# Kernel tuning notes

Hardware: AMD Instinct MI355X
Metric: run time of the kernel (lower is better)

Reference implementation:

```python
import jax, jax.numpy as jnp
import numpy as np

B, S, I, H, O, L = 64, 1024, 512, 512, 512, 3


def setup_inputs() -> dict:
    key = jax.random.key(0)
    ks = jax.random.split(key, 14)
    sc = 0.05  # small init to avoid gate saturation
    inp = {
        "input": jax.random.normal(ks[0], (B, S, I), jnp.float32),
        "hidden_state": jax.random.normal(ks[1], (B, L, H), jnp.float32),
        # gate params; x-side Linear has bias, h-side has none (as in torch module)
        "Wzx": jax.random.normal(ks[2], (L, I, H), jnp.float32) * sc,
        "bzx": jnp.zeros((L, H), jnp.float32),
        "Wzh": jax.random.normal(ks[3], (L, H, H), jnp.float32) * sc,
        "Wrx": jax.random.normal(ks[4], (L, I, H), jnp.float32) * sc,
        "brx": jnp.zeros((L, H), jnp.float32),
        "Wrh": jax.random.normal(ks[5], (L, H, H), jnp.float32) * sc,
        "Wgx": jax.random.normal(ks[6], (L, I, H), jnp.float32) * sc,
        "bgx": jnp.zeros((L, H), jnp.float32),
        "Wgh": jax.random.normal(ks[7], (L, H, H), jnp.float32) * sc,
        "Wout": jax.random.normal(ks[8], (H, O), jnp.float32) * sc,
        "bout": jnp.zeros((O,), jnp.float32),
    }
    return inp


def reference(input, hidden_state, Wzx, bzx, Wzh, Wrx, brx, Wrh, Wgx, bgx, Wgh, Wout, bout):
    n_layers = Wzx.shape[0]
    Bn = input.shape[0]
    Hn = hidden_state.shape[2]
    # layer_states: n_layers initial states + one extra zeros slot (matches torch code)
    states0 = jnp.concatenate(
        [jnp.transpose(hidden_state, (1, 0, 2)),
         jnp.zeros((1, Bn, Hn), input.dtype)], axis=0)  # (L+1, B, H)

    def step(states, x_t):
        x = x_t  # (B, I)
        for l in range(n_layers):
            # NOTE: faithfully reproduces the original's indexing: layer l reads
            # states[l], which for l>=1 was just overwritten by layer l-1 this step.
            h = states[l]
            z = jax.nn.sigmoid(x @ Wzx[l] + bzx[l] + h @ Wzh[l])
            r = jax.nn.sigmoid(x @ Wrx[l] + brx[l] + h @ Wrh[l])
            g = jnp.tanh(x @ Wgx[l] + bgx[l] + (r * h) @ Wgh[l])
            h = z * h + (1.0 - z) * g
            x = h  # dropout=0 -> identity
            states = states.at[l + 1].set(h)
        out_t = x @ Wout + bout  # (B, O)
        return states, out_t

    states_f, outs = jax.lax.scan(step, states0, jnp.transpose(input, (1, 0, 2)))
    layer_output = jnp.transpose(outs, (1, 0, 2))          # (B, S, O)
    hidden_out = jnp.transpose(states_f[:n_layers], (1, 0, 2))  # (B, L, H)
    return layer_output, hidden_out
```

## Files before the change

### kernel.cpp

```cpp
#include <hip/hip_runtime.h>


typedef __attribute__((ext_vector_type(4))) float f32x4;
typedef __attribute__((ext_vector_type(8))) __bf16 bf16x8;

#define NROWS 65536
#define HID_OFF 33554432ull

__device__ __forceinline__ void gload16(const void* g, void* l) {
  __builtin_amdgcn_global_load_lds((const __attribute__((address_space(1))) void*)g,
                                   (__attribute__((address_space(3))) void*)l,
                                   16, 0, 0);
}
__device__ __forceinline__ float sigmoidf_(float x) { return 1.f / (1.f + __expf(-x)); }
__device__ __forceinline__ float tanh_fast(float x) {
  const float e = __expf(2.f * x);
  return 1.f - 2.f / (e + 1.f);
}

__device__ __forceinline__ void stage32(const __bf16* __restrict__ src, int k0,
                                        __bf16* lds, int w, int lane) {
#pragma unroll
  for (int i = 0; i < 2; ++i) {
    const int s0 = (w * 2 + i) * 64;
    const int s = s0 + lane;
    const int row = s >> 2;
    const int cc = (s ^ row) & 3;
    gload16(src + (size_t)row * 512 + k0 + cc * 8, lds + s0 * 8);
  }
}

__device__ __forceinline__ bf16x8 frag32(const __bf16* t, int row, int lane) {
  const int c = ((lane >> 4) ^ row) & 3;
  return *(const bf16x8*)(t + row * 32 + c * 8);
}

__device__ __forceinline__ void stage_ht(const __bf16* __restrict__ src,
                                         __bf16* Ht, int w, int lane) {
#pragma unroll
  for (int i = 0; i < 8; ++i) {
    const int s0 = i * 256 + w * 64;
    const int s = s0 + lane;
    const int row = s >> 4, cc = s & 15;
    gload16(src + (size_t)row * 512 + cc * 8, Ht + s0 * 8);
  }
  asm volatile("s_waitcnt vmcnt(0)");
  __builtin_amdgcn_sched_barrier(0);
  __builtin_amdgcn_s_barrier();
  __builtin_amdgcn_sched_barrier(0);
}

template<int EPI, bool L0>
__global__ __launch_bounds__(256, 4) void gemm7(
    const __bf16* __restrict__ A,
    const __bf16* __restrict__ Bt,
    int tiles_n, int row_off,
    const float* __restrict__ bias,
    const float* __restrict__ cterm,
    const float* __restrict__ h0f,
    const __bf16* __restrict__ haux,
    const __bf16* __restrict__ zf,
    const __bf16* __restrict__ gf,
    __bf16* __restrict__ o_rh,
    __bf16* __restrict__ o_h,
    float* __restrict__ o_f)
{
  __shared__ alignas(16) __bf16 smem[16384];
  __bf16* const A0 = smem;
  __bf16* const B0 = smem + 4096;
  __bf16* const A1 = smem + 8192;
  __bf16* const B1 = smem + 12288;

  const int tid = threadIdx.x, lane = tid & 63, w = tid >> 6;

  int bid = blockIdx.x;
  {
    const int nwg = gridDim.x;
    const int q = nwg >> 3, r = nwg & 7;
    const int x = bid & 7, rest = bid >> 3;
    bid = (x < r ? x * (q + 1) : r * (q + 1) + (x - r) * q) + rest;
  }
  const int tm = bid / tiles_n;
  const int tn = bid - tm * tiles_n;
  const size_t arow0 = (size_t)tm * 128;
  const int brow0 = tn * 128;
  const __bf16* const Ab = A + arow0 * 512;
  const __bf16* const Bb = Bt + (size_t)brow0 * 512;

  const int wr = (w >> 1) * 64;
  const int wc = (w & 1) * 64;

  f32x4 acc[4][4];
  const f32x4 zz = {0.f, 0.f, 0.f, 0.f};
#pragma unroll
  for (int i = 0; i < 4; ++i)
#pragma unroll
    for (int j = 0; j < 4; ++j) acc[i][j] = zz;

  auto step = [&](int t, const __bf16* cA, const __bf16* cB,
                  __bf16* nA, __bf16* nB) {
    if (t < 15) {
      stage32(Ab, (t + 1) * 32, nA, w, lane);
      stage32(Bb, (t + 1) * 32, nB, w, lane);
    }
    bf16x8 af[4], bb4[4];
#pragma unroll
    for (int i = 0; i < 4; ++i) {
      af[i]  = frag32(cA, wr + i * 16 + (lane & 15), lane);
      bb4[i] = frag32(cB, wc + i * 16 + (lane & 15), lane);
    }
#pragma unroll
    for (int mi = 0; mi < 4; ++mi)
#pragma unroll
      for (int ni = 0; ni < 4; ++ni)
        acc[mi][ni] = __builtin_amdgcn_mfma_f32_16x16x32_bf16(af[mi], bb4[ni], acc[mi][ni], 0, 0, 0);
    if (t < 15) {
      asm volatile("s_waitcnt vmcnt(0)");
      __builtin_amdgcn_sched_barrier(0);
    }
    __builtin_amdgcn_sched_barrier(0);
    __builtin_amdgcn_s_barrier();
    __builtin_amdgcn_sched_barrier(0);
  };

  stage32(Ab, 0, A0, w, lane);
  stage32(Bb, 0, B0, w, lane);
  asm volatile("s_waitcnt vmcnt(0)");
  __builtin_amdgcn_sched_barrier(0);
  __builtin_amdgcn_s_barrier();
  __builtin_amdgcn_sched_barrier(0);

#pragma unroll 1
  for (int t = 0; t < 16; t += 2) {
    step(t,     A0, B0, A1, B1);
    step(t + 1, A1, B1, A0, B0);
  }

  const int fcol = lane & 15;
  const int frow = (lane >> 4) * 4;
  const int bb0 = (row_off + (int)arow0) >> 10;

  if (EPI == 0) {
    if (tn < 4) {
      const size_t foff = ((size_t)(tm * 4 + tn)) * 16384 + (size_t)tid * 64;
      __bf16* zw = (__bf16*)zf;
#pragma unroll
      for (int mi = 0; mi < 4; ++mi) {
        bf16x8 p0, p1;
#pragma unroll
        for (int ni = 0; ni < 4; ++ni)
#pragma unroll
          for (int j = 0; j < 4; ++j) {
            const int gcol = brow0 + wc + ni * 16 + fcol;
            float c = acc[mi][ni][j] + bias[gcol];
            if (L0) c += cterm[bb0 * 1024 + gcol];
            const float v = sigmoidf_(c);
            const int idx = ni * 4 + j;
            if (idx < 8) p0[idx] = (__bf16)v; else p1[idx - 8] = (__bf16)v;
          }
        *(bf16x8*)(zw + foff + mi * 16) = p0;
        *(bf16x8*)(zw + foff + mi * 16 + 8) = p1;
      }
    } else if (tn < 8) {
      if (!L0) stage_ht(haux + arow0 * 512 + (tn - 4) * 128, smem, w, lane);
#pragma unroll
      for (int mi = 0; mi < 4; ++mi)
#pragma unroll
        for (int ni = 0; ni < 4; ++ni)
#pragma unroll
          for (int j = 0; j < 4; ++j) {
            const int rloc = (int)arow0 + wr + mi * 16 + frow + j;
            const int gcol = brow0 + wc + ni * 16 + fcol;
            const int nn = gcol - 512;
            float c = acc[mi][ni][j] + bias[gcol];
            if (L0) c += cterm[bb0 * 1024 + gcol];
            const float rv = sigmoidf_(c);
            const float h = L0 ? h0f[bb0 * 1536 + nn]
                               : (float)smem[(wr + mi * 16 + frow + j) * 128 + wc + ni * 16 + fcol];
            o_rh[(size_t)rloc * 512 + nn] = (__bf16)(rv * h);
          }
    } else {
      const size_t foff = ((size_t)(tm * 4 + (tn - 8))) * 16384 + (size_t)tid * 64;
      __bf16* gw = (__bf16*)gf;
#pragma unroll
      for (int mi = 0; mi < 4; ++mi) {
        bf16x8 p0, p1;
#pragma unroll
        for (int ni = 0; ni < 4; ++ni)
#pragma unroll
          for (int j = 0; j < 4; ++j) {
            const int gcol = brow0 + wc + ni * 16 + fcol;
            const float v = acc[mi][ni][j] + bias[gcol];
            const int idx = ni * 4 + j;
            if (idx < 8) p0[idx] = (__bf16)v; else p1[idx - 8] = (__bf16)v;
          }
        *(bf16x8*)(gw + foff + mi * 16) = p0;
        *(bf16x8*)(gw + foff + mi * 16 + 8) = p1;
      }
    }
  } else if (EPI == 1) {
    if (!L0) stage_ht(haux + arow0 * 512 + tn * 128, smem, w, lane);
    const size_t foff = ((size_t)(tm * 4 + tn)) * 16384 + (size_t)tid * 64;
    const bool has_last = (o_f != nullptr) && ((tm & 7) == 7);
#pragma unroll
    for (int mi = 0; mi < 4; ++mi) {
      const bf16x8 z0 = *(const bf16x8*)(zf + foff + mi * 16);
      const bf16x8 z1 = *(const bf16x8*)(zf + foff + mi * 16 + 8);
      const bf16x8 g0 = *(const bf16x8*)(gf + foff + mi * 16);
      const bf16x8 g1 = *(const bf16x8*)(gf + foff + mi * 16 + 8);
#pragma unroll
      for (int ni = 0; ni < 4; ++ni)
#pragma unroll
        for (int j = 0; j < 4; ++j) {
          const int rloc = (int)arow0 + wr + mi * 16 + frow + j;
          const int gcol = brow0 + wc + ni * 16 + fcol;
          const int idx = ni * 4 + j;
          const float zv = (float)(idx < 8 ? z0[idx] : z1[idx - 8]);
          const float gp = (float)(idx < 8 ? g0[idx] : g1[idx - 8]);
          const float gv = tanh_fast(gp + acc[mi][ni][j]);
          const float h = L0 ? h0f[bb0 * 1536 + gcol]
                             : (float)smem[(wr + mi * 16 + frow + j) * 128 + wc + ni * 16 + fcol];
          const float hv = zv * h + (1.f - zv) * gv;
          o_h[(size_t)rloc * 512 + gcol] = (__bf16)hv;
          if (has_last && ((rloc & 1023) == 1023))
            o_f[(size_t)bb0 * 1536 + gcol] = (float)(__bf16)hv;
        }
    }
  } else {
#pragma unroll
    for (int mi = 0; mi < 4; ++mi)
#pragma unroll
      for (int ni = 0; ni < 4; ++ni)
#pragma unroll
        for (int j = 0; j < 4; ++j) {
          const int rloc = (int)arow0 + wr + mi * 16 + frow + j;
          const int gcol = brow0 + wc + ni * 16 + fcol;
          o_f[(size_t)rloc * 512 + gcol] = acc[mi][ni][j] + bias[gcol];
        }
  }
}


__global__ void prep_pack(const float* __restrict__ Wzx, const float* __restrict__ Wzh,
                          const float* __restrict__ Wrx, const float* __restrict__ Wrh,
                          const float* __restrict__ Wgx, const float* __restrict__ Wgh,
                          const float* __restrict__ Wout,
                          __bf16* __restrict__ W1t, __bf16* __restrict__ Wght,
                          __bf16* __restrict__ Woutt)
{
  const int slot = blockIdx.z;
  const float* srcA;
  const float* srcB = nullptr;
  __bf16* dst;
  if (slot < 9) {
    const int l = slot / 3, g = slot % 3;
    srcA = (g == 0 ? Wzx : g == 1 ? Wrx : Wgx) + (size_t)l * 512 * 512;
    if (l > 0 && g < 2) srcB = (g == 0 ? Wzh : Wrh) + (size_t)l * 512 * 512;
    dst = W1t + (size_t)l * 1536 * 512 + (size_t)g * 512 * 512;
  } else if (slot < 12) {
    const int l = slot - 9;
    srcA = Wgh + (size_t)l * 512 * 512;
    dst = Wght + (size_t)l * 512 * 512;
  } else {
    srcA = Wout;
    dst = Woutt;
  }
  __shared__ float tile[32][33];
  const int k0 = blockIdx.x * 32;
  const int n0 = blockIdx.y * 32;
  const int tx = threadIdx.x;
  const int ty = threadIdx.y;
  for (int i = ty; i < 32; i += 8) {
    float v = srcA[(size_t)(k0 + i) * 512 + n0 + tx];
    if (srcB) v += srcB[(size_t)(k0 + i) * 512 + n0 + tx];
    tile[i][tx] = v;
  }
  __syncthreads();
  for (int i = ty; i < 32; i += 8)
    dst[(size_t)(n0 + i) * 512 + k0 + tx] = (__bf16)tile[tx][i];
}

__global__ void cterm_kernel(const float* __restrict__ hidden,
                             const float* __restrict__ Wzh,
                             const float* __restrict__ Wrh,
                             float* __restrict__ Cterm)
{
  const int idx = blockIdx.x * blockDim.x + threadIdx.x;
  const int b = idx >> 10;
  const int n = idx & 1023;
  const float* W = (n < 512 ? Wzh : Wrh);
  const int nn = n & 511;
  const float* h0 = hidden + (size_t)b * 1536;
  float acc = 0.f;
  for (int k = 0; k < 512; ++k) acc += h0[k] * W[(size_t)k * 512 + nn];
  Cterm[idx] = acc;
}

__global__ void small_prep(const float* __restrict__ bzx, const float* __restrict__ brx,
                           const float* __restrict__ bgx, const float* __restrict__ hidden,
                           float* __restrict__ bias1, float* __restrict__ out_hidden)
{
  const int idx = blockIdx.x * blockDim.x + threadIdx.x;
  if (idx < 3 * 1536) {
    const int l = idx / 1536, j = idx % 1536;
    const float* src = (j < 512 ? bzx : j < 1024 ? brx : bgx);
    bias1[idx] = src[l * 512 + (j & 511)];
  }
  const int hidx = idx - 3 * 1536;
  if (hidx >= 0 && hidx < 64 * 512) {
    const int b = hidx >> 9, n = hidx & 511;
    out_hidden[(size_t)b * 1536 + n] = hidden[(size_t)b * 1536 + n];
  }
}

__global__ void convert_x(const float* __restrict__ src, __bf16* __restrict__ dst, long n)
{
  const long i = ((long)blockIdx.x * blockDim.x + threadIdx.x) * 8;
  if (i >= n) return;
  const f32x4 a = *(const f32x4*)(src + i);
  const f32x4 b = *(const f32x4*)(src + i + 4);
  bf16x8 o;
  o[0] = (__bf16)a[0]; o[1] = (__bf16)a[1]; o[2] = (__bf16)a[2]; o[3] = (__bf16)a[3];
  o[4] = (__bf16)b[0]; o[5] = (__bf16)b[1]; o[6] = (__bf16)b[2]; o[7] = (__bf16)b[3];
  *(bf16x8*)(dst + i) = o;
}

extern "C" void kernel_launch(void* const* d_in, const int* in_sizes, int n_in,
                              void* d_out, int out_size, void* d_ws, size_t ws_size,
                              hipStream_t stream) {
  const float* input  = (const float*)d_in[0];
  const float* hidden = (const float*)d_in[1];
  const float* Wzx = (const float*)d_in[2];
  const float* bzx = (const float*)d_in[3];
  const float* Wzh = (const float*)d_in[4];
  const float* Wrx = (const float*)d_in[5];
  const float* brx = (const float*)d_in[6];
  const float* Wrh = (const float*)d_in[7];
  const float* Wgx = (const float*)d_in[8];
  const float* bgx = (const float*)d_in[9];
  const float* Wgh = (const float*)d_in[10];
  const float* Wout = (const float*)d_in[11];
  const float* bout = (const float*)d_in[12];

  float* out = (float*)d_out;
  float* out_hidden = out + HID_OFF;

  char* ws = (char*)d_ws;
  size_t off = 0;
  auto carve = [&](size_t bytes) -> void* {
    off = (off + 255) & ~(size_t)255;
    void* p = ws + off;
    off += bytes;
    return p;
  };

  __bf16* W1t   = (__bf16*)carve(3ull * 1536 * 512 * 2);
  __bf16* Wght  = (__bf16*)carve(3ull * 512 * 512 * 2);
  __bf16* Woutt = (__bf16*)carve(512ull * 512 * 2);
  float*  bias1 = (float*) carve(3ull * 1536 * 4);
  float*  Cterm = (float*) carve(64ull * 1024 * 4);
  const size_t fixed_end = off;

  long chunk_rows = NROWS;
  int C = 1;
  while (C < 32) {
    const size_t need = ((fixed_end + 255) & ~(size_t)255) +
                        5ull * (size_t)chunk_rows * 512 * 2 + 5 * 256;
    if (need <= ws_size) break;
    C *= 2;
    chunk_rows /= 2;
  }
  __bf16* bufA  = (__bf16*)carve((size_t)chunk_rows * 512 * 2);
  __bf16* bufB  = (__bf16*)carve((size_t)chunk_rows * 512 * 2);
  __bf16* zfrag = (__bf16*)carve((size_t)chunk_rows * 512 * 2);
  __bf16* rhb   = (__bf16*)carve((size_t)chunk_rows * 512 * 2);
  __bf16* gfrag = (__bf16*)carve((size_t)chunk_rows * 512 * 2);

  small_prep<<<(3 * 1536 + 64 * 512 + 255) / 256, 256, 0, stream>>>(
      bzx, brx, bgx, hidden, bias1, out_hidden);
  dim3 tp_grid(16, 16, 13), tp_blk(32, 8);
  prep_pack<<<tp_grid, tp_blk, 0, stream>>>(Wzx, Wzh, Wrx, Wrh, Wgx, Wgh, Wout,
                                            W1t, Wght, Woutt);
  cterm_kernel<<<65536 / 256, 256, 0, stream>>>(hidden, Wzh, Wrh, Cterm);

  for (int c = 0; c < C; ++c) {
    const long row_off = (long)c * chunk_rows;
    const long nelem = chunk_rows * 512;
    const int mt = (int)(chunk_rows / 128);

    convert_x<<<(int)((nelem / 8 + 255) / 256), 256, 0, stream>>>(
        input + (size_t)row_off * 512, bufA, nelem);

    gemm7<0, true><<<mt * 12, 256, 0, stream>>>(
        bufA, W1t, 12, (int)row_off, bias1, Cterm, hidden, nullptr,
        zfrag, gfrag, rhb, nullptr, nullptr);
    gemm7<1, true><<<mt * 4, 256, 0, stream>>>(
        rhb, Wght, 4, (int)row_off, nullptr, nullptr, hidden, nullptr,
        zfrag, gfrag, nullptr, bufB, out_hidden + 512);

    gemm7<0, false><<<mt * 12, 256, 0, stream>>>(
        bufB, W1t + 1536 * 512, 12, (int)row_off, bias1 + 1536, nullptr, nullptr, bufB,
        zfrag, gfrag, rhb, nullptr, nullptr);
    gemm7<1, false><<<mt * 4, 256, 0, stream>>>(
        rhb, Wght + 512 * 512, 4, (int)row_off, nullptr, nullptr, nullptr, bufB,
        zfrag, gfrag, nullptr, bufA, out_hidden + 1024);

    gemm7<0, false><<<mt * 12, 256, 0, stream>>>(
        bufA, W1t + 2 * 1536 * 512, 12, (int)row_off, bias1 + 3072, nullptr, nullptr, bufA,
        zfrag, gfrag, rhb, nullptr, nullptr);
    gemm7<1, false><<<mt * 4, 256, 0, stream>>>(
        rhb, Wght + 2 * 512 * 512, 4, (int)row_off, nullptr, nullptr, nullptr, bufA,
        zfrag, gfrag, nullptr, bufB, nullptr);

    gemm7<2, false><<<mt * 4, 256, 0, stream>>>(
        bufB, Woutt, 4, (int)row_off, bout, nullptr, nullptr, nullptr,
        nullptr, nullptr, nullptr, nullptr, out + (size_t)row_off * 512);
  }
}
```

Before: 927.5 us.

## Triple-buffer GEMM K-loop with two-ahead prefetch and new LDS swizzle

Replaces the double-buffered LDS staging in the bf16 MFMA GEMM with a three-buffer ring that prefetches two K-slices ahead and waits with vmcnt(4) rather than draining all loads every step. The XOR swizzle for the A/B tiles now uses row>>1 to change the LDS bank pattern. The EPI==1 epilogue issues its z/g fragment loads before staging the hidden tile, so those loads overlap. In exchange, LDS use grows from 32KB to 48KB per block and launch bounds drop to 3 blocks per CU, which lowers occupancy.

After: 863.1 us (median of 3 runs). -6.9%, faster.

```diff
diff --git a/kernel.cpp b/kernel.cpp
--- a/kernel.cpp
+++ b/kernel.cpp
@@ -25,13 +25,13 @@
     const int s0 = (w * 2 + i) * 64;
     const int s = s0 + lane;
     const int row = s >> 2;
-    const int cc = (s ^ row) & 3;
+    const int cc = ((s & 3) ^ (row >> 1)) & 3;
     gload16(src + (size_t)row * 512 + k0 + cc * 8, lds + s0 * 8);
   }
 }
 
 __device__ __forceinline__ bf16x8 frag32(const __bf16* t, int row, int lane) {
-  const int c = ((lane >> 4) ^ row) & 3;
+  const int c = (((lane >> 4) ^ (row >> 1)) & 3);
   return *(const bf16x8*)(t + row * 32 + c * 8);
 }
 
@@ -51,7 +51,7 @@
 }
 
 template<int EPI, bool L0>
-__global__ __launch_bounds__(256, 4) void gemm7(
+__global__ __launch_bounds__(256, 3) void gemm9(
     const __bf16* __restrict__ A,
     const __bf16* __restrict__ Bt,
     int tiles_n, int row_off,
@@ -65,11 +65,13 @@
     __bf16* __restrict__ o_h,
     float* __restrict__ o_f)
 {
-  __shared__ alignas(16) __bf16 smem[16384];
+  __shared__ alignas(16) __bf16 smem[24576];
   __bf16* const A0 = smem;
   __bf16* const B0 = smem + 4096;
   __bf16* const A1 = smem + 8192;
   __bf16* const B1 = smem + 12288;
+  __bf16* const A2 = smem + 16384;
+  __bf16* const B2 = smem + 20480;
 
   const int tid = threadIdx.x, lane = tid & 63, w = tid >> 6;
 
@@ -97,11 +99,11 @@
 #pragma unroll
     for (int j = 0; j < 4; ++j) acc[i][j] = zz;
 
-  auto step = [&](int t, const __bf16* cA, const __bf16* cB,
-                  __bf16* nA, __bf16* nB) {
-    if (t < 15) {
-      stage32(Ab, (t + 1) * 32, nA, w, lane);
-      stage32(Bb, (t + 1) * 32, nB, w, lane);
+  auto stepf = [&](int t, const __bf16* cA, const __bf16* cB,
+                   __bf16* nA, __bf16* nB, int vm) {
+    if (nA) {
+      stage32(Ab, (t + 2) * 32, nA, w, lane);
+      stage32(Bb, (t + 2) * 32, nB, w, lane);
     }
     bf16x8 af[4], bb4[4];
 #pragma unroll
@@ -114,27 +116,37 @@
 #pragma unroll
       for (int ni = 0; ni < 4; ++ni)
         acc[mi][ni] = __builtin_amdgcn_mfma_f32_16x16x32_bf16(af[mi], bb4[ni], acc[mi][ni], 0, 0, 0);
-    if (t < 15) {
+    if (vm == 4) {
+      asm volatile("s_waitcnt vmcnt(4)");
+      __builtin_amdgcn_sched_barrier(0);
+    } else if (vm == 0) {
       asm volatile("s_waitcnt vmcnt(0)");
       __builtin_amdgcn_sched_barrier(0);
     }
-    __builtin_amdgcn_sched_barrier(0);
     __builtin_amdgcn_s_barrier();
     __builtin_amdgcn_sched_barrier(0);
   };
 
   stage32(Ab, 0, A0, w, lane);
   stage32(Bb, 0, B0, w, lane);
-  asm volatile("s_waitcnt vmcnt(0)");
+  stage32(Ab, 32, A1, w, lane);
+  stage32(Bb, 32, B1, w, lane);
+  asm volatile("s_waitcnt vmcnt(4)");
   __builtin_amdgcn_sched_barrier(0);
   __builtin_amdgcn_s_barrier();
   __builtin_amdgcn_sched_barrier(0);
 
 #pragma unroll 1
-  for (int t = 0; t < 16; t += 2) {
-    step(t,     A0, B0, A1, B1);
-    step(t + 1, A1, B1, A0, B0);
-  }
+  for (int it = 0; it < 4; ++it) {
+    const int t = it * 3;
+    stepf(t,     A0, B0, A2, B2, 4);
+    stepf(t + 1, A1, B1, A0, B0, 4);
+    stepf(t + 2, A2, B2, A1, B1, 4);
+  }
+  stepf(12, A0, B0, A2, B2, 4);
+  stepf(13, A1, B1, A0, B0, 4);
+  stepf(14, A2, B2, nullptr, nullptr, 0);
+  stepf(15, A0, B0, nullptr, nullptr, -1);
 
   const int fcol = lane & 15;
   const int frow = (lane >> 4) * 4;
@@ -199,15 +211,19 @@
       }
     }
   } else if (EPI == 1) {
+    const size_t foff = ((size_t)(tm * 4 + tn)) * 16384 + (size_t)tid * 64;
+    bf16x8 zr[4][2], gr[4][2];
+#pragma unroll
+    for (int mi = 0; mi < 4; ++mi) {
+      zr[mi][0] = *(const bf16x8*)(zf + foff + mi * 16);
+      zr[mi][1] = *(const bf16x8*)(zf + foff + mi * 16 + 8);
+      gr[mi][0] = *(const bf16x8*)(gf + foff + mi * 16);
+      gr[mi][1] = *(const bf16x8*)(gf + foff + mi * 16 + 8);
+    }
     if (!L0) stage_ht(haux + arow0 * 512 + tn * 128, smem, w, lane);
-    const size_t foff = ((size_t)(tm * 4 + tn)) * 16384 + (size_t)tid * 64;
     const bool has_last = (o_f != nullptr) && ((tm & 7) == 7);
 #pragma unroll
     for (int mi = 0; mi < 4; ++mi) {
-      const bf16x8 z0 = *(const bf16x8*)(zf + foff + mi * 16);
-      const bf16x8 z1 = *(const bf16x8*)(zf + foff + mi * 16 + 8);
-      const bf16x8 g0 = *(const bf16x8*)(gf + foff + mi * 16);
-      const bf16x8 g1 = *(const bf16x8*)(gf + foff + mi * 16 + 8);
 #pragma unroll
       for (int ni = 0; ni < 4; ++ni)
 #pragma unroll
@@ -215,8 +231,8 @@
           const int rloc = (int)arow0 + wr + mi * 16 + frow + j;
           const int gcol = brow0 + wc + ni * 16 + fcol;
           const int idx = ni * 4 + j;
-          const float zv = (float)(idx < 8 ? z0[idx] : z1[idx - 8]);
-          const float gp = (float)(idx < 8 ? g0[idx] : g1[idx - 8]);
+          const float zv = (float)(idx < 8 ? zr[mi][0][idx] : zr[mi][1][idx - 8]);
+          const float gp = (float)(idx < 8 ? gr[mi][0][idx] : gr[mi][1][idx - 8]);
           const float gv = tanh_fast(gp + acc[mi][ni][j]);
           const float h = L0 ? h0f[bb0 * 1536 + gcol]
                              : (float)smem[(wr + mi * 16 + frow + j) * 128 + wc + ni * 16 + fcol];
@@ -391,28 +407,28 @@
     convert_x<<<(int)((nelem / 8 + 255) / 256), 256, 0, stream>>>(
         input + (size_t)row_off * 512, bufA, nelem);
 
-    gemm7<0, true><<<mt * 12, 256, 0, stream>>>(
+    gemm9<0, true><<<mt * 12, 256, 0, stream>>>(
         bufA, W1t, 12, (int)row_off, bias1, Cterm, hidden, nullptr,
         zfrag, gfrag, rhb, nullptr, nullptr);
-    gemm7<1, true><<<mt * 4, 256, 0, stream>>>(
+    gemm9<1, true><<<mt * 4, 256, 0, stream>>>(
         rhb, Wght, 4, (int)row_off, nullptr, nullptr, hidden, nullptr,
         zfrag, gfrag, nullptr, bufB, out_hidden + 512);
 
-    gemm7<0, false><<<mt * 12, 256, 0, stream>>>(
+    gemm9<0, false><<<mt * 12, 256, 0, stream>>>(
         bufB, W1t + 1536 * 512, 12, (int)row_off, bias1 + 1536, nullptr, nullptr, bufB,
         zfrag, gfrag, rhb, nullptr, nullptr);
-    gemm7<1, false><<<mt * 4, 256, 0, stream>>>(
+    gemm9<1, false><<<mt * 4, 256, 0, stream>>>(
         rhb, Wght + 512 * 512, 4, (int)row_off, nullptr, nullptr, nullptr, bufB,
         zfrag, gfrag, nullptr, bufA, out_hidden + 1024);
 
-    gemm7<0, false><<<mt * 12, 256, 0, stream>>>(
+    gemm9<0, false><<<mt * 12, 256, 0, stream>>>(
         bufA, W1t + 2 * 1536 * 512, 12, (int)row_off, bias1 + 3072, nullptr, nullptr, bufA,
         zfrag, gfrag, rhb, nullptr, nullptr);
-    gemm7<1, false><<<mt * 4, 256, 0, stream>>>(
+    gemm9<1, false><<<mt * 4, 256, 0, stream>>>(
         rhb, Wght + 2 * 512 * 512, 4, (int)row_off, nullptr, nullptr, nullptr, bufA,
         zfrag, gfrag, nullptr, bufB, nullptr);
 
-    gemm7<2, false><<<mt * 4, 256, 0, stream>>>(
+    gemm9<2, false><<<mt * 4, 256, 0, stream>>>(
         bufB, Woutt, 4, (int)row_off, bout, nullptr, nullptr, nullptr,
         nullptr, nullptr, nullptr, nullptr, out + (size_t)row_off * 512);
   }
```

## Use 256x256 tiles with 16-wave blocks, triple-buffered LDS, and h-fragment passthrough

Applied to the files above, without the earlier changes.

Replaces the 128x128 GEMM tile with 256 threads by a 256x256 tile computed by 1024 threads, with a three-stage LDS pipeline that waits on vmcnt(2) to keep two K-slices in flight. The r-gate epilogue now stages h through LDS in two passes and writes h in fragment order to a new hfrag buffer, so the update GEMM reads h directly instead of restaging it from global memory. The goal is higher operand reuse per loaded byte and less epilogue staging, at the cost of one block per CU, 96KB LDS per block, fewer blocks in total (possible wave-quantisation and occupancy loss), and an extra workspace buffer.

After: 1.312 ms. 41.5% more time.

```diff
diff --git a/kernel.cpp b/kernel.cpp
--- a/kernel.cpp
+++ b/kernel.cpp
@@ -18,28 +18,24 @@
   return 1.f - 2.f / (e + 1.f);
 }
 
-__device__ __forceinline__ void stage32(const __bf16* __restrict__ src, int k0,
-                                        __bf16* lds, int w, int lane) {
-#pragma unroll
-  for (int i = 0; i < 2; ++i) {
-    const int s0 = (w * 2 + i) * 64;
-    const int s = s0 + lane;
-    const int row = s >> 2;
-    const int cc = (s ^ row) & 3;
-    gload16(src + (size_t)row * 512 + k0 + cc * 8, lds + s0 * 8);
-  }
+__device__ __forceinline__ void stage256(const __bf16* __restrict__ src, int k0,
+                                         __bf16* lds, int w, int lane) {
+  const int s = w * 64 + lane;
+  const int row = s >> 2;
+  const int cc = ((s & 3) ^ (row >> 1)) & 3;
+  gload16(src + (size_t)row * 512 + k0 + cc * 8, lds + (w * 64) * 8);
 }
 
 __device__ __forceinline__ bf16x8 frag32(const __bf16* t, int row, int lane) {
-  const int c = ((lane >> 4) ^ row) & 3;
+  const int c = (((lane >> 4) ^ (row >> 1)) & 3);
   return *(const bf16x8*)(t + row * 32 + c * 8);
 }
 
-__device__ __forceinline__ void stage_ht(const __bf16* __restrict__ src,
-                                         __bf16* Ht, int w, int lane) {
-#pragma unroll
-  for (int i = 0; i < 8; ++i) {
-    const int s0 = i * 256 + w * 64;
+__device__ __forceinline__ void stage_ht256(const __bf16* __restrict__ src,
+                                            __bf16* Ht, int w, int lane) {
+#pragma unroll
+  for (int i = 0; i < 4; ++i) {
+    const int s0 = i * 1024 + w * 64;
     const int s = s0 + lane;
     const int row = s >> 4, cc = s & 15;
     gload16(src + (size_t)row * 512 + cc * 8, Ht + s0 * 8);
@@ -51,7 +47,7 @@
 }
 
 template<int EPI, bool L0>
-__global__ __launch_bounds__(256, 4) void gemm7(
+__global__ __launch_bounds__(1024, 1) void gemm14(
     const __bf16* __restrict__ A,
     const __bf16* __restrict__ Bt,
     int tiles_n, int row_off,
@@ -61,17 +57,21 @@
     const __bf16* __restrict__ haux,
     const __bf16* __restrict__ zf,
     const __bf16* __restrict__ gf,
+    const __bf16* __restrict__ hf,
     __bf16* __restrict__ o_rh,
     __bf16* __restrict__ o_h,
     float* __restrict__ o_f)
 {
-  __shared__ alignas(16) __bf16 smem[16384];
+  __shared__ alignas(16) __bf16 smem[49152];
   __bf16* const A0 = smem;
-  __bf16* const B0 = smem + 4096;
-  __bf16* const A1 = smem + 8192;
-  __bf16* const B1 = smem + 12288;
+  __bf16* const B0 = smem + 8192;
+  __bf16* const A1 = smem + 16384;
+  __bf16* const B1 = smem + 24576;
+  __bf16* const A2 = smem + 32768;
+  __bf16* const B2 = smem + 40960;
 
   const int tid = threadIdx.x, lane = tid & 63, w = tid >> 6;
+  const int wm = w >> 2, wn = w & 3;
 
   int bid = blockIdx.x;
   {
@@ -82,14 +82,11 @@
   }
   const int tm = bid / tiles_n;
   const int tn = bid - tm * tiles_n;
-  const size_t arow0 = (size_t)tm * 128;
-  const int brow0 = tn * 128;
+  const size_t arow0 = (size_t)tm * 256;
+  const int brow0 = tn * 256;
   const __bf16* const Ab = A + arow0 * 512;
   const __bf16* const Bb = Bt + (size_t)brow0 * 512;
 
-  const int wr = (w >> 1) * 64;
-  const int wc = (w & 1) * 64;
-
   f32x4 acc[4][4];
   const f32x4 zz = {0.f, 0.f, 0.f, 0.f};
 #pragma unroll
@@ -97,52 +94,63 @@
 #pragma unroll
     for (int j = 0; j < 4; ++j) acc[i][j] = zz;
 
-  auto step = [&](int t, const __bf16* cA, const __bf16* cB,
-                  __bf16* nA, __bf16* nB) {
-    if (t < 15) {
-      stage32(Ab, (t + 1) * 32, nA, w, lane);
-      stage32(Bb, (t + 1) * 32, nB, w, lane);
+  auto stepf = [&](int kst, const __bf16* cA, const __bf16* cB,
+                   __bf16* nA, __bf16* nB, int vm) {
+    if (nA) {
+      stage256(Ab, kst, nA, w, lane);
+      stage256(Bb, kst, nB, w, lane);
     }
-    bf16x8 af[4], bb4[4];
+    bf16x8 af[4], bf_[4];
 #pragma unroll
     for (int i = 0; i < 4; ++i) {
-      af[i]  = frag32(cA, wr + i * 16 + (lane & 15), lane);
-      bb4[i] = frag32(cB, wc + i * 16 + (lane & 15), lane);
+      af[i]  = frag32(cA, wm * 64 + i * 16 + (lane & 15), lane);
+      bf_[i] = frag32(cB, wn * 64 + i * 16 + (lane & 15), lane);
     }
 #pragma unroll
     for (int mi = 0; mi < 4; ++mi)
 #pragma unroll
       for (int ni = 0; ni < 4; ++ni)
-        acc[mi][ni] = __builtin_amdgcn_mfma_f32_16x16x32_bf16(af[mi], bb4[ni], acc[mi][ni], 0, 0, 0);
-    if (t < 15) {
+        acc[mi][ni] = __builtin_amdgcn_mfma_f32_16x16x32_bf16(af[mi], bf_[ni], acc[mi][ni], 0, 0, 0);
+    if (vm == 2) {
+      asm volatile("s_waitcnt vmcnt(2)");
+      __builtin_amdgcn_sched_barrier(0);
+    } else if (vm == 0) {
       asm volatile("s_waitcnt vmcnt(0)");
       __builtin_amdgcn_sched_barrier(0);
     }
-    __builtin_amdgcn_sched_barrier(0);
     __builtin_amdgcn_s_barrier();
     __builtin_amdgcn_sched_barrier(0);
   };
 
-  stage32(Ab, 0, A0, w, lane);
-  stage32(Bb, 0, B0, w, lane);
-  asm volatile("s_waitcnt vmcnt(0)");
+  stage256(Ab, 0, A0, w, lane);
+  stage256(Bb, 0, B0, w, lane);
+  stage256(Ab, 32, A1, w, lane);
+  stage256(Bb, 32, B1, w, lane);
+  asm volatile("s_waitcnt vmcnt(2)");
   __builtin_amdgcn_sched_barrier(0);
   __builtin_amdgcn_s_barrier();
   __builtin_amdgcn_sched_barrier(0);
 
 #pragma unroll 1
-  for (int t = 0; t < 16; t += 2) {
-    step(t,     A0, B0, A1, B1);
-    step(t + 1, A1, B1, A0, B0);
-  }
+  for (int it = 0; it < 4; ++it) {
+    const int kb = it * 96;
+    stepf(kb + 64,  A0, B0, A2, B2, 2);
+    stepf(kb + 96,  A1, B1, A0, B0, 2);
+    stepf(kb + 128, A2, B2, A1, B1, 2);
+  }
+  stepf(14 * 32, A0, B0, A2, B2, 2);
+  stepf(15 * 32, A1, B1, A0, B0, 2);
+  stepf(0,       A2, B2, nullptr, nullptr, 0);
+  stepf(0,       A0, B0, nullptr, nullptr, -1);
+  __builtin_amdgcn_s_barrier();
 
   const int fcol = lane & 15;
   const int frow = (lane >> 4) * 4;
   const int bb0 = (row_off + (int)arow0) >> 10;
 
   if (EPI == 0) {
-    if (tn < 4) {
-      const size_t foff = ((size_t)(tm * 4 + tn)) * 16384 + (size_t)tid * 64;
+    if (tn < 2) {
+      const size_t foff = ((size_t)(tm * 2 + tn)) * 65536 + (size_t)tid * 64;
       __bf16* zw = (__bf16*)zf;
 #pragma unroll
       for (int mi = 0; mi < 4; ++mi) {
@@ -151,7 +159,7 @@
         for (int ni = 0; ni < 4; ++ni)
 #pragma unroll
           for (int j = 0; j < 4; ++j) {
-            const int gcol = brow0 + wc + ni * 16 + fcol;
+            const int gcol = brow0 + wn * 64 + ni * 16 + fcol;
             float c = acc[mi][ni][j] + bias[gcol];
             if (L0) c += cterm[bb0 * 1024 + gcol];
             const float v = sigmoidf_(c);
@@ -161,26 +169,58 @@
         *(bf16x8*)(zw + foff + mi * 16) = p0;
         *(bf16x8*)(zw + foff + mi * 16 + 8) = p1;
       }
-    } else if (tn < 8) {
-      if (!L0) stage_ht(haux + arow0 * 512 + (tn - 4) * 128, smem, w, lane);
-#pragma unroll
-      for (int mi = 0; mi < 4; ++mi)
-#pragma unroll
-        for (int ni = 0; ni < 4; ++ni)
-#pragma unroll
-          for (int j = 0; j < 4; ++j) {
-            const int rloc = (int)arow0 + wr + mi * 16 + frow + j;
-            const int gcol = brow0 + wc + ni * 16 + fcol;
-            const int nn = gcol - 512;
-            float c = acc[mi][ni][j] + bias[gcol];
-            if (L0) c += cterm[bb0 * 1024 + gcol];
-            const float rv = sigmoidf_(c);
-            const float h = L0 ? h0f[bb0 * 1536 + nn]
-                               : (float)smem[(wr + mi * 16 + frow + j) * 128 + wc + ni * 16 + fcol];
-            o_rh[(size_t)rloc * 512 + nn] = (__bf16)(rv * h);
+    } else if (tn < 4) {
+      const int u = tn - 2;
+      const size_t foffh = ((size_t)(tm * 2 + u)) * 65536 + (size_t)tid * 64;
+      __bf16* hw = (__bf16*)hf;
+      if (L0) {
+#pragma unroll
+        for (int mi = 0; mi < 4; ++mi)
+#pragma unroll
+          for (int ni = 0; ni < 4; ++ni)
+#pragma unroll
+            for (int j = 0; j < 4; ++j) {
+              const int rloc = (int)arow0 + wm * 64 + mi * 16 + frow + j;
+              const int gcol = brow0 + wn * 64 + ni * 16 + fcol;
+              const int nn = gcol - 512;
+              float c = acc[mi][ni][j] + bias[gcol] + cterm[bb0 * 1024 + gcol];
+              const float rv = sigmoidf_(c);
+              const float h = h0f[bb0 * 1536 + nn];
+              o_rh[(size_t)rloc * 512 + nn] = (__bf16)(rv * h);
+            }
+      } else {
+#pragma unroll 1
+        for (int p = 0; p < 2; ++p) {
+          __syncthreads();
+          stage_ht256(haux + arow0 * 512 + u * 256 + p * 128, smem, w, lane);
+          if (((w >> 1) & 1) == p) {
+#pragma unroll
+            for (int mi = 0; mi < 4; ++mi) {
+              bf16x8 h0v, h1v;
+#pragma unroll
+              for (int ni = 0; ni < 4; ++ni)
+#pragma unroll
+                for (int j = 0; j < 4; ++j) {
+                  const int rloc = (int)arow0 + wm * 64 + mi * 16 + frow + j;
+                  const int gcol = brow0 + wn * 64 + ni * 16 + fcol;
+                  const int nn = gcol - 512;
+                  float c = acc[mi][ni][j] + bias[gcol];
+                  const float rv = sigmoidf_(c);
+                  const int lr = wm * 64 + mi * 16 + frow + j;
+                  const int lc = (w & 1) * 64 + ni * 16 + fcol;
+                  const __bf16 hb = smem[lr * 128 + lc];
+                  o_rh[(size_t)rloc * 512 + nn] = (__bf16)(rv * (float)hb);
+                  const int idx = ni * 4 + j;
+                  if (idx < 8) h0v[idx] = hb; else h1v[idx - 8] = hb;
+                }
+              *(bf16x8*)(hw + foffh + mi * 16) = h0v;
+              *(bf16x8*)(hw + foffh + mi * 16 + 8) = h1v;
+            }
           }
+        }
+      }
     } else {
-      const size_t foff = ((size_t)(tm * 4 + (tn - 8))) * 16384 + (size_t)tid * 64;
+      const size_t foff = ((size_t)(tm * 2 + (tn - 4))) * 65536 + (size_t)tid * 64;
       __bf16* gw = (__bf16*)gf;
 #pragma unroll
       for (int mi = 0; mi < 4; ++mi) {
@@ -189,7 +229,7 @@
         for (int ni = 0; ni < 4; ++ni)
 #pragma unroll
           for (int j = 0; j < 4; ++j) {
-            const int gcol = brow0 + wc + ni * 16 + fcol;
+            const int gcol = brow0 + wn * 64 + ni * 16 + fcol;
             const float v = acc[mi][ni][j] + bias[gcol];
             const int idx = ni * 4 + j;
             if (idx < 8) p0[idx] = (__bf16)v; else p1[idx - 8] = (__bf16)v;
@@ -199,27 +239,31 @@
       }
     }
   } else if (EPI == 1) {
-    if (!L0) stage_ht(haux + arow0 * 512 + tn * 128, smem, w, lane);
-    const size_t foff = ((size_t)(tm * 4 + tn)) * 16384 + (size_t)tid * 64;
-    const bool has_last = (o_f != nullptr) && ((tm & 7) == 7);
+    const size_t foff = ((size_t)(tm * 2 + tn)) * 65536 + (size_t)tid * 64;
+    const bool has_last = (o_f != nullptr) && ((tm & 3) == 3);
 #pragma unroll
     for (int mi = 0; mi < 4; ++mi) {
       const bf16x8 z0 = *(const bf16x8*)(zf + foff + mi * 16);
       const bf16x8 z1 = *(const bf16x8*)(zf + foff + mi * 16 + 8);
       const bf16x8 g0 = *(const bf16x8*)(gf + foff + mi * 16);
       const bf16x8 g1 = *(const bf16x8*)(gf + foff + mi * 16 + 8);
+      bf16x8 h0v, h1v;
+      if (!L0) {
+        h0v = *(const bf16x8*)(hf + foff + mi * 16);
+        h1v = *(const bf16x8*)(hf + foff + mi * 16 + 8);
+      }
 #pragma unroll
       for (int ni = 0; ni < 4; ++ni)
 #pragma unroll
         for (int j = 0; j < 4; ++j) {
-          const int rloc = (int)arow0 + wr + mi * 16 + frow + j;
-          const int gcol = brow0 + wc + ni * 16 + fcol;
+          const int rloc = (int)arow0 + wm * 64 + mi * 16 + frow + j;
+          const int gcol = brow0 + wn * 64 + ni * 16 + fcol;
           const int idx = ni * 4 + j;
           const float zv = (float)(idx < 8 ? z0[idx] : z1[idx - 8]);
           const float gp = (float)(idx < 8 ? g0[idx] : g1[idx - 8]);
           const float gv = tanh_fast(gp + acc[mi][ni][j]);
           const float h = L0 ? h0f[bb0 * 1536 + gcol]
-                             : (float)smem[(wr + mi * 16 + frow + j) * 128 + wc + ni * 16 + fcol];
+                             : (float)(idx < 8 ? h0v[idx] : h1v[idx - 8]);
           const float hv = zv * h + (1.f - zv) * gv;
           o_h[(size_t)rloc * 512 + gcol] = (__bf16)hv;
           if (has_last && ((rloc & 1023) == 1023))
@@ -233,8 +277,8 @@
       for (int ni = 0; ni < 4; ++ni)
 #pragma unroll
         for (int j = 0; j < 4; ++j) {
-          const int rloc = (int)arow0 + wr + mi * 16 + frow + j;
-          const int gcol = brow0 + wc + ni * 16 + fcol;
+          const int rloc = (int)arow0 + wm * 64 + mi * 16 + frow + j;
+          const int gcol = brow0 + wn * 64 + ni * 16 + fcol;
           o_f[(size_t)rloc * 512 + gcol] = acc[mi][ni][j] + bias[gcol];
         }
   }
@@ -365,7 +409,7 @@
   int C = 1;
   while (C < 32) {
     const size_t need = ((fixed_end + 255) & ~(size_t)255) +
-                        5ull * (size_t)chunk_rows * 512 * 2 + 5 * 256;
+                        6ull * (size_t)chunk_rows * 512 * 2 + 6 * 256;
     if (need <= ws_size) break;
     C *= 2;
     chunk_rows /= 2;
@@ -375,6 +419,7 @@
   __bf16* zfrag = (__bf16*)carve((size_t)chunk_rows * 512 * 2);
   __bf16* rhb   = (__bf16*)carve((size_t)chunk_rows * 512 * 2);
   __bf16* gfrag = (__bf16*)carve((size_t)chunk_rows * 512 * 2);
+  __bf16* hfrag = (__bf16*)carve((size_t)chunk_rows * 512 * 2);
 
   small_prep<<<(3 * 1536 + 64 * 512 + 255) / 256, 256, 0, stream>>>(
       bzx, brx, bgx, hidden, bias1, out_hidden);
@@ -386,34 +431,34 @@
   for (int c = 0; c < C; ++c) {
     const long row_off = (long)c * chunk_rows;
     const long nelem = chunk_rows * 512;
-    const int mt = (int)(chunk_rows / 128);
+    const int mt2 = (int)(chunk_rows / 256);
 
     convert_x<<<(int)((nelem / 8 + 255) / 256), 256, 0, stream>>>(
         input + (size_t)row_off * 512, bufA, nelem);
 
-    gemm7<0, true><<<mt * 12, 256, 0, stream>>>(
-        bufA, W1t, 12, (int)row_off, bias1, Cterm, hidden, nullptr,
-        zfrag, gfrag, rhb, nullptr, nullptr);
-    gemm7<1, true><<<mt * 4, 256, 0, stream>>>(
-        rhb, Wght, 4, (int)row_off, nullptr, nullptr, hidden, nullptr,
-        zfrag, gfrag, nullptr, bufB, out_hidden + 512);
-
-    gemm7<0, false><<<mt * 12, 256, 0, stream>>>(
-        bufB, W1t + 1536 * 512, 12, (int)row_off, bias1 + 1536, nullptr, nullptr, bufB,
-        zfrag, gfrag, rhb, nullptr, nullptr);
-    gemm7<1, false><<<mt * 4, 256, 0, stream>>>(
-        rhb, Wght + 512 * 512, 4, (int)row_off, nullptr, nullptr, nullptr, bufB,
-        zfrag, gfrag, nullptr, bufA, out_hidden + 1024);
-
-    gemm7<0, false><<<mt * 12, 256, 0, stream>>>(
-        bufA, W1t + 2 * 1536 * 512, 12, (int)row_off, bias1 + 3072, nullptr, nullptr, bufA,
-        zfrag, gfrag, rhb, nullptr, nullptr);
-    gemm7<1, false><<<mt * 4, 256, 0, stream>>>(
-        rhb, Wght + 2 * 512 * 512, 4, (int)row_off, nullptr, nullptr, nullptr, bufA,
-        zfrag, gfrag, nullptr, bufB, nullptr);
-
-    gemm7<2, false><<<mt * 4, 256, 0, stream>>>(
-        bufB, Woutt, 4, (int)row_off, bout, nullptr, nullptr, nullptr,
-        nullptr, nullptr, nullptr, nullptr, out + (size_t)row_off * 512);
-  }
-}
+    gemm14<0, true><<<mt2 * 6, 1024, 0, stream>>>(
+        bufA, W1t, 6, (int)row_off, bias1, Cterm, hidden, nullptr,
+        zfrag, gfrag, hfrag, rhb, nullptr, nullptr);
+    gemm14<1, true><<<mt2 * 2, 1024, 0, stream>>>(
+        rhb, Wght, 2, (int)row_off, nullptr, nullptr, hidden, nullptr,
+        zfrag, gfrag, hfrag, nullptr, bufB, out_hidden + 512);
+
+    gemm14<0, false><<<mt2 * 6, 1024, 0, stream>>>(
+        bufB, W1t + 1536 * 512, 6, (int)row_off, bias1 + 1536, nullptr, nullptr, bufB,
+        zfrag, gfrag, hfrag, rhb, nullptr, nullptr);
+    gemm14<1, false><<<mt2 * 2, 1024, 0, stream>>>(
+        rhb, Wght + 512 * 512, 2, (int)row_off, nullptr, nullptr, nullptr, nullptr,
+        zfrag, gfrag, hfrag, nullptr, bufA, out_hidden + 1024);
+
+    gemm14<0, false><<<mt2 * 6, 1024, 0, stream>>>(
+        bufA, W1t + 2 * 1536 * 512, 6, (int)row_off, bias1 + 3072, nullptr, nullptr, bufA,
+        zfrag, gfrag, hfrag, rhb, nullptr, nullptr);
+    gemm14<1, false><<<mt2 * 2, 1024, 0, stream>>>(
+        rhb, Wght + 2 * 512 * 512, 2, (int)row_off, nullptr, nullptr, nullptr, nullptr,
+        zfrag, gfrag, hfrag, nullptr, bufB, nullptr);
+
+    gemm14<2, false><<<mt2 * 2, 1024, 0, stream>>>(
+        bufB, Woutt, 2, (int)row_off, bout, nullptr, nullptr, nullptr,
+        nullptr, nullptr, nullptr, nullptr, nullptr, out + (size_t)row_off * 512);
+  }
+}
```
